# Performance work log

Hardware: AMD Instinct MI355X
Metric: run time of the kernel (lower is better)

## Reference

```python
import jax, jax.numpy as jnp
import numpy as np

TEMPERATURE = 0.1
B, D, A = 8192, 256, 4


def setup_inputs() -> dict:
    key = jax.random.key(0)
    k1, k2 = jax.random.split(key)
    # scale by 1/sqrt(D) so dot products are O(1) and exp(sim/T) is finite
    embeddings = jax.random.normal(k1, (B, D), dtype=jnp.float32) / jnp.sqrt(jnp.float32(D))
    labels = jax.random.randint(k2, (B, A), 0, 6, dtype=jnp.int64)
    return {"embeddings": embeddings, "labels": labels}


def reference(embeddings, labels):
    b = embeddings.shape[0]
    # [B, B] similarity scaled by temperature
    sim = jnp.matmul(embeddings, embeddings.T) / TEMPERATURE
    # positive mask: ANY aspect matches (vectorized over aspects), diagonal zeroed
    pos_mask = jnp.any(labels[:, None, :] == labels[None, :, :], axis=-1)
    pos_mask = pos_mask & ~jnp.eye(b, dtype=bool)
    pos_mask = pos_mask.astype(sim.dtype)

    exp_sim = jnp.exp(sim)
    positive_sim = jnp.sum(exp_sim * pos_mask, axis=1)            # [B]
    all_sim = jnp.sum(exp_sim, axis=1) - jnp.diagonal(exp_sim)   # [B]

    valid = positive_sim > 0
    pos_safe = jnp.where(valid, positive_sim, 1.0)
    all_safe = jnp.where(valid, all_sim, 1.0)
    row_loss = jnp.where(valid, -jnp.log(pos_safe / (all_safe + 1e-8)), 0.0)

    num_pos = jnp.sum(valid.astype(sim.dtype))
    loss = jnp.where(num_pos > 0, jnp.sum(row_loss) / jnp.maximum(num_pos, 1.0), 0.0)
    return loss
```

## Files before the change

### kernel.cpp

```cpp
#include <hip/hip_runtime.h>
#include <stdint.h>

typedef short short8 __attribute__((ext_vector_type(8)));
typedef float f32x4 __attribute__((ext_vector_type(4)));
typedef float f32x2 __attribute__((ext_vector_type(2)));

#define B_TOTAL 8192
#define DDIM 256
#define BM 128
#define BN 64
#define NSPLIT 16
#define COLS_PER (B_TOTAL / NSPLIT)
#define ITERS (COLS_PER / BN)
#define NBLOCKS ((B_TOTAL / BM) * NSPLIT)
#define SCALE_HALF 3.79828546f
#define LN2F 0.6931471805599453f

typedef __attribute__((address_space(3))) char lds_char;
typedef __attribute__((address_space(1))) const char gbl_char;

__device__ __forceinline__ unsigned short f2bf(float f) {
  unsigned int u = __builtin_bit_cast(unsigned int, f);
  u = (u + 0x7FFFu + ((u >> 16) & 1u)) >> 16;
  return (unsigned short)u;
}

__global__ __launch_bounds__(256) void prep_all(
    const float* __restrict__ E, const int* __restrict__ lab,
    unsigned short* __restrict__ Eb, unsigned int* __restrict__ plab,
    float* __restrict__ posAll) {
  const int t = blockIdx.x * 256 + threadIdx.x;
  const float4* s4 = (const float4*)E + (size_t)t * 2;
  float4 v0 = s4[0], v1 = s4[1];
  short8 o;
  o[0] = (short)f2bf(v0.x * SCALE_HALF); o[1] = (short)f2bf(v0.y * SCALE_HALF);
  o[2] = (short)f2bf(v0.z * SCALE_HALF); o[3] = (short)f2bf(v0.w * SCALE_HALF);
  o[4] = (short)f2bf(v1.x * SCALE_HALF); o[5] = (short)f2bf(v1.y * SCALE_HALF);
  o[6] = (short)f2bf(v1.z * SCALE_HALF); o[7] = (short)f2bf(v1.w * SCALE_HALF);
  *(short8*)(Eb + (size_t)t * 8) = o;
  if (t < B_TOTAL) {
    int4 l = ((const int4*)lab)[t];
    plab[t] = (1u << ((unsigned)l.x & 31u))
            | (1u << (((unsigned)l.y & 31u) + 6u))
            | (1u << (((unsigned)l.z & 31u) + 12u))
            | (1u << (((unsigned)l.w & 31u) + 18u));
  }
  if (t < 2 * B_TOTAL) posAll[t] = 0.0f;
}

struct __align__(16) SMem {
  char btile[2][BN * DDIM * 2];
  unsigned int plab_all[COLS_PER];
};

template <int DIAG>
__device__ __forceinline__ void do_epilogue(
    const f32x4 (&acc)[4][2], int colbase, int it, int l15,
    const unsigned int (&pi)[2][4], const int (&irow)[2][4],
    const unsigned int* plab_all, f32x2 (&pos2)[2][2], f32x2 (&all2)[2][2]) {
#pragma unroll
  for (int n = 0; n < 4; ++n) {
    const int j = colbase + n * 16 + l15;
    const unsigned int hj = plab_all[it * BN + n * 16 + l15];
#pragma unroll
    for (int m = 0; m < 2; ++m) {
      float e[4];
#pragma unroll
      for (int q = 0; q < 4; ++q) {
        float v = __builtin_amdgcn_exp2f(acc[n][m][q]);
        if (DIAG) { if (j == irow[m][q]) v = 0.0f; }
        e[q] = v;
      }
      f32x2 p01 = { (pi[m][0] & hj) ? e[0] : 0.0f, (pi[m][1] & hj) ? e[1] : 0.0f };
      f32x2 p23 = { (pi[m][2] & hj) ? e[2] : 0.0f, (pi[m][3] & hj) ? e[3] : 0.0f };
      all2[m][0] += (f32x2){e[0], e[1]};
      all2[m][1] += (f32x2){e[2], e[3]};
      pos2[m][0] += p01;
      pos2[m][1] += p23;
    }
  }
}

__global__ __launch_bounds__(256, 2) void main_kernel(
    const unsigned short* __restrict__ Eb, const unsigned int* __restrict__ plab,
    float* __restrict__ posArr, float* __restrict__ allArr) {
  __shared__ SMem sm;
  const int tid = threadIdx.x;
  const int lane = tid & 63;
  const int wid = tid >> 6;
  const int l15 = lane & 15;
  const int l4 = lane >> 4;
  const int rb = (int)blockIdx.x & 63;
  const int cs = (int)blockIdx.x >> 6;
  const int rowbase = rb * BM;
  const int colstart = cs * COLS_PER;

  auto stage = [&](int bufi, int cb) {
#pragma unroll
    for (int q = 0; q < 8; ++q) {
      const unsigned int L = (unsigned int)wid * 8192u + (unsigned int)q * 1024u +
                             (unsigned int)lane * 16u;
      const unsigned int r = L >> 9;
      const unsigned int s = (L >> 4) & 31u;
      const unsigned int c = s ^ (r & 7u);
      const char* src = (const char*)(Eb + (size_t)(cb + (int)r) * DDIM + c * 8);
      char* dst = sm.btile[bufi] + (unsigned int)wid * 8192u + (unsigned int)q * 1024u;
      __builtin_amdgcn_global_load_lds((gbl_char*)src, (lds_char*)dst, 16, 0, 0);
    }
  };

  stage(0, colstart);

  short8 afrag[2][8];
#pragma unroll
  for (int m = 0; m < 2; ++m) {
    const int row = rowbase + wid * 32 + m * 16 + l15;
    const unsigned short* rp = Eb + (size_t)row * DDIM + l4 * 8;
#pragma unroll
    for (int k = 0; k < 8; ++k) afrag[m][k] = *(const short8*)(rp + k * 32);
  }

  {
    unsigned int a0 = plab[colstart + tid];
    unsigned int a1 = plab[colstart + 256 + tid];
    sm.plab_all[tid] = a0;
    sm.plab_all[tid + 256] = a1;
  }

  unsigned int pi[2][4];
  int irow[2][4];
#pragma unroll
  for (int m = 0; m < 2; ++m)
#pragma unroll
    for (int q = 0; q < 4; ++q) {
      const int i = rowbase + wid * 32 + m * 16 + l4 * 4 + q;
      irow[m][q] = i;
      pi[m][q] = plab[i];
    }

  asm volatile("s_waitcnt lgkmcnt(0)" ::: "memory");
  __builtin_amdgcn_sched_barrier(0);

  f32x2 pos2[2][2] = {};
  f32x2 all2[2][2] = {};

  for (int it = 0; it < ITERS; ++it) {
    const int colbase = colstart + it * BN;
    const int cur = it & 1;

    if (it + 1 < ITERS) {
      stage(cur ^ 1, colbase + BN);
      asm volatile("s_waitcnt vmcnt(8)" ::: "memory");
    } else {
      asm volatile("s_waitcnt vmcnt(0)" ::: "memory");
    }
    __builtin_amdgcn_s_barrier();
    __builtin_amdgcn_sched_barrier(0);

    f32x4 acc[4][2];
#pragma unroll
    for (int n = 0; n < 4; ++n)
#pragma unroll
      for (int m = 0; m < 2; ++m) acc[n][m] = (f32x4){0.f, 0.f, 0.f, 0.f};

    __builtin_amdgcn_s_setprio(1);
#pragma unroll
    for (int k = 0; k < 8; ++k) {
      short8 b[4];
#pragma unroll
      for (int n = 0; n < 4; ++n) {
        const unsigned int rr = (unsigned int)(n * 16 + l15);
        const unsigned int cdx = (unsigned int)(k * 4 + l4);
        const unsigned int s = cdx ^ (rr & 7u);
        b[n] = *(const short8*)(sm.btile[cur] + rr * 512u + s * 16u);
      }
#pragma unroll
      for (int n = 0; n < 4; ++n)
#pragma unroll
        for (int m = 0; m < 2; ++m)
          acc[n][m] = __builtin_amdgcn_mfma_f32_16x16x32_bf16(
              afrag[m][k], b[n], acc[n][m], 0, 0, 0);
    }
    __builtin_amdgcn_s_setprio(0);

    const bool hasDiag = (colbase < rowbase + BM) && (rowbase < colbase + BN);
    if (hasDiag)
      do_epilogue<1>(acc, colbase, it, l15, pi, irow, sm.plab_all, pos2, all2);
    else
      do_epilogue<0>(acc, colbase, it, l15, pi, irow, sm.plab_all, pos2, all2);

    __builtin_amdgcn_s_barrier();
    __builtin_amdgcn_sched_barrier(0);
  }

#pragma unroll
  for (int m = 0; m < 2; ++m)
#pragma unroll
    for (int q = 0; q < 4; ++q) {
      float p = pos2[m][q >> 1][q & 1], al = all2[m][q >> 1][q & 1];
      p += __shfl_xor(p, 1); p += __shfl_xor(p, 2);
      p += __shfl_xor(p, 4); p += __shfl_xor(p, 8);
      al += __shfl_xor(al, 1); al += __shfl_xor(al, 2);
      al += __shfl_xor(al, 4); al += __shfl_xor(al, 8);
      if (l15 == 0) {
        atomicAdd(&posArr[irow[m][q]], p);
        atomicAdd(&allArr[irow[m][q]], al);
      }
    }
}

__global__ __launch_bounds__(1024) void finalize_kernel(
    const float* __restrict__ posArr, const float* __restrict__ allArr,
    float* __restrict__ out) {
  float ls = 0.f, cnt = 0.f;
#pragma unroll
  for (int k = 0; k < B_TOTAL / 1024; ++k) {
    const int i = threadIdx.x + (k << 10);
    const float p = posArr[i];
    const float a = allArr[i];
    if (p > 0.f) {
      ls += (__builtin_amdgcn_logf(a + 1e-8f) - __builtin_amdgcn_logf(p)) * LN2F;
      cnt += 1.f;
    }
  }
#pragma unroll
  for (int msk = 1; msk < 64; msk <<= 1) {
    ls += __shfl_xor(ls, msk);
    cnt += __shfl_xor(cnt, msk);
  }
  __shared__ float sls[16], scnt[16];
  const int w = threadIdx.x >> 6;
  if ((threadIdx.x & 63) == 0) { sls[w] = ls; scnt[w] = cnt; }
  __syncthreads();
  if (threadIdx.x == 0) {
    float L = 0.f, C = 0.f;
    for (int i = 0; i < 16; ++i) { L += sls[i]; C += scnt[i]; }
    out[0] = (C > 0.f) ? L / fmaxf(C, 1.f) : 0.f;
  }
}

extern "C" void kernel_launch(void* const* d_in, const int* in_sizes, int n_in,
                              void* d_out, int out_size, void* d_ws, size_t ws_size,
                              hipStream_t stream) {
  const float* E = (const float*)d_in[0];
  const int* lab = (const int*)d_in[1];
  float* out = (float*)d_out;
  char* ws = (char*)d_ws;

  unsigned short* Eb = (unsigned short*)ws;
  unsigned int* plab = (unsigned int*)(ws + 4u * 1024u * 1024u);
  float* posArr = (float*)(ws + 4u * 1024u * 1024u + 32u * 1024u);
  float* allArr = posArr + B_TOTAL;

  prep_all<<<1024, 256, 0, stream>>>(E, lab, Eb, plab, posArr);
  main_kernel<<<NBLOCKS, 256, 0, stream>>>(Eb, plab, posArr, allArr);
  finalize_kernel<<<1, 1024, 0, stream>>>(posArr, allArr, out);
}
```

Before: 108.7 us.

## Double row tile to 256 rows per block with two-half column processing

Each block now covers 256 rows instead of 128, and each wave holds four 16-row A fragments, so every B tile staged in LDS is reused across twice as many rows. The 64-column tile is processed in two 32-column halves, which keeps the accumulator count unchanged while the A fragments and per-row state double. This halves the total B tile traffic from global memory and LDS. It also halves the block count to 512 and raises register pressure, which could hurt occupancy under the 2-blocks-per-SM launch bound.

```diff
diff --git a/kernel.cpp b/kernel.cpp
--- a/kernel.cpp
+++ b/kernel.cpp
@@ -7,7 +7,7 @@
 
 #define B_TOTAL 8192
 #define DDIM 256
-#define BM 128
+#define BM 256
 #define BN 64
 #define NSPLIT 16
 #define COLS_PER (B_TOTAL / NSPLIT)
@@ -55,20 +55,21 @@
 
 template <int DIAG>
 __device__ __forceinline__ void do_epilogue(
-    const f32x4 (&acc)[4][2], int colbase, int it, int l15,
-    const unsigned int (&pi)[2][4], const int (&irow)[2][4],
-    const unsigned int* plab_all, f32x2 (&pos2)[2][2], f32x2 (&all2)[2][2]) {
-#pragma unroll
-  for (int n = 0; n < 4; ++n) {
-    const int j = colbase + n * 16 + l15;
-    const unsigned int hj = plab_all[it * BN + n * 16 + l15];
-#pragma unroll
-    for (int m = 0; m < 2; ++m) {
+    const f32x4 (&acc)[2][4], int jbase , int lbase ,
+    int l15, int row0 ,
+    const unsigned int (&pi)[4][4], const unsigned int* plab_all,
+    f32x2 (&pos2)[4][2], f32x2 (&all2)[4][2]) {
+#pragma unroll
+  for (int n2 = 0; n2 < 2; ++n2) {
+    const int j = jbase + n2 * 16 + l15;
+    const unsigned int hj = plab_all[lbase + n2 * 16 + l15];
+#pragma unroll
+    for (int m = 0; m < 4; ++m) {
       float e[4];
 #pragma unroll
       for (int q = 0; q < 4; ++q) {
-        float v = __builtin_amdgcn_exp2f(acc[n][m][q]);
-        if (DIAG) { if (j == irow[m][q]) v = 0.0f; }
+        float v = __builtin_amdgcn_exp2f(acc[n2][m][q]);
+        if (DIAG) { if (j == row0 + m * 16 + q) v = 0.0f; }
         e[q] = v;
       }
       f32x2 p01 = { (pi[m][0] & hj) ? e[0] : 0.0f, (pi[m][1] & hj) ? e[1] : 0.0f };
@@ -90,10 +91,11 @@
   const int wid = tid >> 6;
   const int l15 = lane & 15;
   const int l4 = lane >> 4;
-  const int rb = (int)blockIdx.x & 63;
-  const int cs = (int)blockIdx.x >> 6;
+  const int rb = (int)blockIdx.x & 31;
+  const int cs = (int)blockIdx.x >> 5;
   const int rowbase = rb * BM;
   const int colstart = cs * COLS_PER;
+  const int row0 = rowbase + wid * 64 + l4 * 4;
 
   auto stage = [&](int bufi, int cb) {
 #pragma unroll
@@ -111,10 +113,10 @@
 
   stage(0, colstart);
 
-  short8 afrag[2][8];
-#pragma unroll
-  for (int m = 0; m < 2; ++m) {
-    const int row = rowbase + wid * 32 + m * 16 + l15;
+  short8 afrag[4][8];
+#pragma unroll
+  for (int m = 0; m < 4; ++m) {
+    const int row = rowbase + wid * 64 + m * 16 + l15;
     const unsigned short* rp = Eb + (size_t)row * DDIM + l4 * 8;
 #pragma unroll
     for (int k = 0; k < 8; ++k) afrag[m][k] = *(const short8*)(rp + k * 32);
@@ -127,22 +129,17 @@
     sm.plab_all[tid + 256] = a1;
   }
 
-  unsigned int pi[2][4];
-  int irow[2][4];
-#pragma unroll
-  for (int m = 0; m < 2; ++m)
-#pragma unroll
-    for (int q = 0; q < 4; ++q) {
-      const int i = rowbase + wid * 32 + m * 16 + l4 * 4 + q;
-      irow[m][q] = i;
-      pi[m][q] = plab[i];
-    }
+  unsigned int pi[4][4];
+#pragma unroll
+  for (int m = 0; m < 4; ++m)
+#pragma unroll
+    for (int q = 0; q < 4; ++q) pi[m][q] = plab[row0 + m * 16 + q];
 
   asm volatile("s_waitcnt lgkmcnt(0)" ::: "memory");
   __builtin_amdgcn_sched_barrier(0);
 
-  f32x2 pos2[2][2] = {};
-  f32x2 all2[2][2] = {};
+  f32x2 pos2[4][2] = {};
+  f32x2 all2[4][2] = {};
 
   for (int it = 0; it < ITERS; ++it) {
     const int colbase = colstart + it * BN;
@@ -157,44 +154,50 @@
     __builtin_amdgcn_s_barrier();
     __builtin_amdgcn_sched_barrier(0);
 
-    f32x4 acc[4][2];
-#pragma unroll
-    for (int n = 0; n < 4; ++n)
-#pragma unroll
-      for (int m = 0; m < 2; ++m) acc[n][m] = (f32x4){0.f, 0.f, 0.f, 0.f};
-
-    __builtin_amdgcn_s_setprio(1);
-#pragma unroll
-    for (int k = 0; k < 8; ++k) {
-      short8 b[4];
-#pragma unroll
-      for (int n = 0; n < 4; ++n) {
-        const unsigned int rr = (unsigned int)(n * 16 + l15);
-        const unsigned int cdx = (unsigned int)(k * 4 + l4);
-        const unsigned int s = cdx ^ (rr & 7u);
-        b[n] = *(const short8*)(sm.btile[cur] + rr * 512u + s * 16u);
+    const bool hasDiag = (colbase < rowbase + BM) && (rowbase < colbase + BN);
+
+#pragma unroll
+    for (int nh = 0; nh < 2; ++nh) {
+      f32x4 acc[2][4];
+#pragma unroll
+      for (int n2 = 0; n2 < 2; ++n2)
+#pragma unroll
+        for (int m = 0; m < 4; ++m) acc[n2][m] = (f32x4){0.f, 0.f, 0.f, 0.f};
+
+      __builtin_amdgcn_s_setprio(1);
+#pragma unroll
+      for (int k = 0; k < 8; ++k) {
+        short8 b[2];
+#pragma unroll
+        for (int n2 = 0; n2 < 2; ++n2) {
+          const unsigned int rr = (unsigned int)(nh * 32 + n2 * 16 + l15);
+          const unsigned int cdx = (unsigned int)(k * 4 + l4);
+          const unsigned int s = cdx ^ (rr & 7u);
+          b[n2] = *(const short8*)(sm.btile[cur] + rr * 512u + s * 16u);
+        }
+#pragma unroll
+        for (int n2 = 0; n2 < 2; ++n2)
+#pragma unroll
+          for (int m = 0; m < 4; ++m)
+            acc[n2][m] = __builtin_amdgcn_mfma_f32_16x16x32_bf16(
+                afrag[m][k], b[n2], acc[n2][m], 0, 0, 0);
       }
-#pragma unroll
-      for (int n = 0; n < 4; ++n)
-#pragma unroll
-        for (int m = 0; m < 2; ++m)
-          acc[n][m] = __builtin_amdgcn_mfma_f32_16x16x32_bf16(
-              afrag[m][k], b[n], acc[n][m], 0, 0, 0);
-    }
-    __builtin_amdgcn_s_setprio(0);
-
-    const bool hasDiag = (colbase < rowbase + BM) && (rowbase < colbase + BN);
-    if (hasDiag)
-      do_epilogue<1>(acc, colbase, it, l15, pi, irow, sm.plab_all, pos2, all2);
-    else
-      do_epilogue<0>(acc, colbase, it, l15, pi, irow, sm.plab_all, pos2, all2);
+      __builtin_amdgcn_s_setprio(0);
+
+      if (hasDiag)
+        do_epilogue<1>(acc, colbase + nh * 32, it * BN + nh * 32, l15, row0,
+                       pi, sm.plab_all, pos2, all2);
+      else
+        do_epilogue<0>(acc, colbase + nh * 32, it * BN + nh * 32, l15, row0,
+                       pi, sm.plab_all, pos2, all2);
+    }
 
     __builtin_amdgcn_s_barrier();
     __builtin_amdgcn_sched_barrier(0);
   }
 
 #pragma unroll
-  for (int m = 0; m < 2; ++m)
+  for (int m = 0; m < 4; ++m)
 #pragma unroll
     for (int q = 0; q < 4; ++q) {
       float p = pos2[m][q >> 1][q & 1], al = all2[m][q >> 1][q & 1];
@@ -203,8 +206,8 @@
       al += __shfl_xor(al, 1); al += __shfl_xor(al, 2);
       al += __shfl_xor(al, 4); al += __shfl_xor(al, 8);
       if (l15 == 0) {
-        atomicAdd(&posArr[irow[m][q]], p);
-        atomicAdd(&allArr[irow[m][q]], al);
+        atomicAdd(&posArr[row0 + m * 16 + q], p);
+        atomicAdd(&allArr[row0 + m * 16 + q], al);
       }
     }
 }
```

After: 133.4 us. 1.23x slower.
